# Kernel tuning notes

Measured on AMD Instinct MI355X. Metric: run time of the kernel, lower is better.

The kernel has to match this reference:

```python
import jax, jax.numpy as jnp
import numpy as np

N_NODES = 50000
N_EDGES = 400000


def setup_inputs() -> dict:
    key = jax.random.key(0)
    ks = jax.random.split(key, 8)
    d_in, d_hid, d_out = 512, 512, 256
    feats = jax.random.normal(ks[0], (N_NODES, d_in), dtype=jnp.float32)
    src = jax.random.randint(ks[1], (N_EDGES,), 0, N_NODES, dtype=jnp.int32)
    dst = jax.random.randint(ks[2], (N_EDGES,), 0, N_NODES, dtype=jnp.int32)
    # Glorot-ish scaled weights so activations stay O(1)
    W0 = jax.random.normal(ks[3], (d_in, d_hid), dtype=jnp.float32) / np.sqrt(d_in)
    b0 = jnp.zeros((d_hid,), jnp.float32)
    W1 = jax.random.normal(ks[4], (d_hid, d_hid), dtype=jnp.float32) / np.sqrt(d_hid)
    b1 = jnp.zeros((d_hid,), jnp.float32)
    W2 = jax.random.normal(ks[5], (d_hid, d_out), dtype=jnp.float32) / np.sqrt(d_hid)
    b2 = jnp.zeros((d_out,), jnp.float32)
    return {"feats": feats, "src": src, "dst": dst,
            "W0": W0, "b0": b0, "W1": W1, "b1": b1, "W2": W2, "b2": b2}


def _sage_conv_gcn(h, src, dst, W, b, deg):
    # DGL SAGEConv aggregator_type='gcn':
    # h_neigh[v] = (sum_{u->v} h[u] + h[v]) / (in_deg(v) + 1); out = h_neigh @ W + b
    agg = jax.ops.segment_sum(h[src], dst, num_segments=h.shape[0])  # [N, d]
    h_neigh = (agg + h) / (deg[:, None] + 1.0)
    return h_neigh @ W + b


def reference(feats, src, dst, W0, b0, W1, b1, W2, b2):
    N = feats.shape[0]
    deg = jax.ops.segment_sum(jnp.ones((src.shape[0],), feats.dtype), dst,
                              num_segments=N)  # in-degree per node
    h = jax.nn.relu(_sage_conv_gcn(feats, src, dst, W0, b0, deg))  # dropout p=0, norm none
    h = jax.nn.relu(_sage_conv_gcn(h, src, dst, W1, b1, deg))
    h = _sage_conv_gcn(h, src, dst, W2, b2, deg)  # final layer: no activation
    return h
```

## Files before the change

kernel.cpp:

```cpp
#include <hip/hip_runtime.h>
#include <stdint.h>

#define N_NODES 50000
#define N_EDGES 400000
#define MPAD    50048
#define SCAN_B  49

typedef __bf16 bf16x8 __attribute__((ext_vector_type(8)));
typedef float  f32x4  __attribute__((ext_vector_type(4)));
typedef unsigned short ushort_t;
typedef unsigned int   uint_t;

__device__ __forceinline__ ushort_t f2b(float f){
    uint_t x = __float_as_uint(f);
    x += 0x7FFFu + ((x >> 16) & 1u);
    return (ushort_t)(x >> 16);
}
__device__ __forceinline__ float b2f(ushort_t h){
    return __uint_as_float(((uint_t)h) << 16);
}

__global__ void zero_two(int* a, int* b, int n){
    int i = blockIdx.x * blockDim.x + threadIdx.x;
    if (i < n){ a[i] = 0; b[i] = 0; }
}

__global__ void hist_kernel(const int* __restrict__ dst, int* __restrict__ deg, int E){
    int i = blockIdx.x * blockDim.x + threadIdx.x;
    if (i < E) atomicAdd(&deg[dst[i]], 1);
}

__global__ __launch_bounds__(1024) void blk_scan_kernel(
        const int* __restrict__ deg, int* __restrict__ offs,
        int* __restrict__ bsum, int n){
    __shared__ int buf[1024];
    const int t = threadIdx.x, b = blockIdx.x;
    const int i = b * 1024 + t;
    int v = (i < n) ? deg[i] : 0;
    buf[t] = v; __syncthreads();
    for (int off = 1; off < 1024; off <<= 1){
        int x = (t >= off) ? buf[t - off] : 0;
        __syncthreads();
        buf[t] += x;
        __syncthreads();
    }
    if (i < n) offs[i] = buf[t] - v;
    if (t == 1023) bsum[b] = buf[1023];
}

__global__ void bsum_scan_kernel(int* __restrict__ bsum, int nb){
    int t = threadIdx.x;
    int orig = (t < nb) ? bsum[t] : 0;
    int v = orig;
    #pragma unroll
    for (int off = 1; off < 64; off <<= 1){
        int x = __shfl_up(v, off, 64);
        if (t >= off) v += x;
    }
    if (t < nb) bsum[t] = v - orig;
}

__global__ __launch_bounds__(1024) void add_off_kernel(
        int* __restrict__ offs, const int* __restrict__ bsum, int n){
    int i = blockIdx.x * 1024 + threadIdx.x;
    if (i < n) offs[i] += bsum[blockIdx.x];
    if (i == 0) offs[n] = N_EDGES;
}

__global__ void fill_kernel(const int* __restrict__ src, const int* __restrict__ dst,
                            const int* __restrict__ offs, int* __restrict__ cursor,
                            int* __restrict__ nbr, int E){
    int i = blockIdx.x * blockDim.x + threadIdx.x;
    if (i < E){
        int d = dst[i];
        int p = atomicAdd(&cursor[d], 1);
        nbr[offs[d] + p] = src[i];
    }
}

__global__ void f2b_kernel(const float4* __restrict__ in, ushort4* __restrict__ out, int n4){
    int i = blockIdx.x * blockDim.x + threadIdx.x;
    if (i < n4){
        float4 v = in[i];
        ushort4 o; o.x = f2b(v.x); o.y = f2b(v.y); o.z = f2b(v.z); o.w = f2b(v.w);
        out[i] = o;
    }
}

__global__ void wtrans_kernel(const float* __restrict__ W, ushort_t* __restrict__ Wt,
                              int K, int N){
    int i = blockIdx.x * blockDim.x + threadIdx.x;
    if (i < K * N){
        int n = i / K, k = i - n * K;
        Wt[i] = f2b(W[k * N + n]);
    }
}

__device__ __forceinline__ void load16(const void* g, void* l){
    __builtin_amdgcn_global_load_lds((const __attribute__((address_space(1))) void*)g,
                                     (__attribute__((address_space(3))) void*)l, 16, 0, 0);
}

__global__ __launch_bounds__(256, 2) void gemm_bt(const ushort_t* __restrict__ A,
                                                  const ushort_t* __restrict__ Bt,
                                                  ushort_t* __restrict__ C,
                                                  int N, int K){
    __shared__ ushort_t As[128 * 32];
    __shared__ ushort_t Bs[256 * 32];
    const int tid  = threadIdx.x, lane = tid & 63, wave = tid >> 6;
    const int bm = blockIdx.x, bn = blockIdx.y;
    const int fr = lane & 15;
    const int fk = (lane >> 4) * 8;
    const int wm = (wave >> 1) * 64, wn = (wave & 1) * 128;
    f32x4 acc[4][8] = {};

    for (int kt = 0; kt < K; kt += 32){
        __syncthreads();
        #pragma unroll
        for (int i = 0; i < 2; i++){
            int s = tid + i * 256;
            load16(A + (size_t)(bm * 128 + (s >> 2)) * K + kt + (s & 3) * 8,
                   (char*)As + s * 16);
        }
        #pragma unroll
        for (int i = 0; i < 4; i++){
            int s = tid + i * 256;
            load16(Bt + (size_t)(bn * 256 + (s >> 2)) * K + kt + (s & 3) * 8,
                   (char*)Bs + s * 16);
        }
        __syncthreads();
        bf16x8 af[4], bf[8];
        #pragma unroll
        for (int t = 0; t < 4; t++)
            af[t] = *(const bf16x8*)(const void*)(As + (wm + t * 16 + fr) * 32 + fk);
        #pragma unroll
        for (int t = 0; t < 8; t++)
            bf[t] = *(const bf16x8*)(const void*)(Bs + (wn + t * 16 + fr) * 32 + fk);
        #pragma unroll
        for (int tm = 0; tm < 4; tm++)
            #pragma unroll
            for (int tn = 0; tn < 8; tn++)
                acc[tm][tn] = __builtin_amdgcn_mfma_f32_16x16x32_bf16(
                                  af[tm], bf[tn], acc[tm][tn], 0, 0, 0);
    }
    const int r0 = (lane >> 4) * 4, c0 = lane & 15;
    #pragma unroll
    for (int tm = 0; tm < 4; tm++){
        #pragma unroll
        for (int tn = 0; tn < 8; tn++){
            int rbase = bm * 128 + wm + tm * 16 + r0;
            int cidx  = bn * 256 + wn + tn * 16 + c0;
            #pragma unroll
            for (int reg = 0; reg < 4; reg++)
                C[(size_t)(rbase + reg) * N + cidx] = f2b(acc[tm][tn][reg]);
        }
    }
}

__device__ __forceinline__ void acc8(float* a, uint4 y){
    a[0] += b2f((ushort_t)(y.x & 0xffff)); a[1] += b2f((ushort_t)(y.x >> 16));
    a[2] += b2f((ushort_t)(y.y & 0xffff)); a[3] += b2f((ushort_t)(y.y >> 16));
    a[4] += b2f((ushort_t)(y.z & 0xffff)); a[5] += b2f((ushort_t)(y.z >> 16));
    a[6] += b2f((ushort_t)(y.w & 0xffff)); a[7] += b2f((ushort_t)(y.w >> 16));
}
__device__ __forceinline__ void acc4(float* a, uint2 y){
    a[0] += b2f((ushort_t)(y.x & 0xffff)); a[1] += b2f((ushort_t)(y.x >> 16));
    a[2] += b2f((ushort_t)(y.y & 0xffff)); a[3] += b2f((ushort_t)(y.y >> 16));
}

__global__ __launch_bounds__(256) void agg_relu_kernel(
        const ushort_t* __restrict__ Y, const int* __restrict__ offs,
        const int* __restrict__ nbr, const float* __restrict__ bias,
        ushort_t* __restrict__ H){
    const int lane = threadIdx.x & 63, wave = threadIdx.x >> 6;
    const int v = blockIdx.x * 4 + wave;
    const int off = lane * 8;
    float a[8];
    {   uint4 y = *(const uint4*)(const void*)(Y + (size_t)v * 512 + off);
        a[0] = b2f((ushort_t)(y.x & 0xffff)); a[1] = b2f((ushort_t)(y.x >> 16));
        a[2] = b2f((ushort_t)(y.y & 0xffff)); a[3] = b2f((ushort_t)(y.y >> 16));
        a[4] = b2f((ushort_t)(y.z & 0xffff)); a[5] = b2f((ushort_t)(y.z >> 16));
        a[6] = b2f((ushort_t)(y.w & 0xffff)); a[7] = b2f((ushort_t)(y.w >> 16)); }
    const int beg = offs[v], end = offs[v + 1];
    int i = beg;
    for (; i + 8 <= end; i += 8){
        uint4 yy[8];
        #pragma unroll
        for (int j = 0; j < 8; j++){
            int u = nbr[i + j];
            yy[j] = *(const uint4*)(const void*)(Y + (size_t)u * 512 + off);
        }
        #pragma unroll
        for (int j = 0; j < 8; j++) acc8(a, yy[j]);
    }
    for (; i + 4 <= end; i += 4){
        uint4 yy[4];
        #pragma unroll
        for (int j = 0; j < 4; j++){
            int u = nbr[i + j];
            yy[j] = *(const uint4*)(const void*)(Y + (size_t)u * 512 + off);
        }
        #pragma unroll
        for (int j = 0; j < 4; j++) acc8(a, yy[j]);
    }
    for (; i < end; i++){
        int u = nbr[i];
        uint4 y = *(const uint4*)(const void*)(Y + (size_t)u * 512 + off);
        acc8(a, y);
    }
    const float inv = 1.0f / (float)(end - beg + 1);
    float4 bb0 = ((const float4*)bias)[lane * 2];
    float4 bb1 = ((const float4*)bias)[lane * 2 + 1];
    float r[8];
    r[0] = a[0]*inv + bb0.x; r[1] = a[1]*inv + bb0.y;
    r[2] = a[2]*inv + bb0.z; r[3] = a[3]*inv + bb0.w;
    r[4] = a[4]*inv + bb1.x; r[5] = a[5]*inv + bb1.y;
    r[6] = a[6]*inv + bb1.z; r[7] = a[7]*inv + bb1.w;
    #pragma unroll
    for (int j = 0; j < 8; j++) r[j] = r[j] > 0.f ? r[j] : 0.f;
    uint4 o;
    o.x = (uint_t)f2b(r[0]) | ((uint_t)f2b(r[1]) << 16);
    o.y = (uint_t)f2b(r[2]) | ((uint_t)f2b(r[3]) << 16);
    o.z = (uint_t)f2b(r[4]) | ((uint_t)f2b(r[5]) << 16);
    o.w = (uint_t)f2b(r[6]) | ((uint_t)f2b(r[7]) << 16);
    *(uint4*)(void*)(H + (size_t)v * 512 + off) = o;
}

__global__ __launch_bounds__(256) void agg_out_kernel(
        const ushort_t* __restrict__ Y, const int* __restrict__ offs,
        const int* __restrict__ nbr, const float* __restrict__ bias,
        float* __restrict__ out){
    const int lane = threadIdx.x & 63, wave = threadIdx.x >> 6;
    const int v = blockIdx.x * 4 + wave;
    const int off = lane * 4;
    float a[4];
    {   uint2 y = *(const uint2*)(const void*)(Y + (size_t)v * 256 + off);
        a[0] = b2f((ushort_t)(y.x & 0xffff)); a[1] = b2f((ushort_t)(y.x >> 16));
        a[2] = b2f((ushort_t)(y.y & 0xffff)); a[3] = b2f((ushort_t)(y.y >> 16)); }
    const int beg = offs[v], end = offs[v + 1];
    int i = beg;
    for (; i + 8 <= end; i += 8){
        uint2 yy[8];
        #pragma unroll
        for (int j = 0; j < 8; j++){
            int u = nbr[i + j];
            yy[j] = *(const uint2*)(const void*)(Y + (size_t)u * 256 + off);
        }
        #pragma unroll
        for (int j = 0; j < 8; j++) acc4(a, yy[j]);
    }
    for (; i + 4 <= end; i += 4){
        uint2 yy[4];
        #pragma unroll
        for (int j = 0; j < 4; j++){
            int u = nbr[i + j];
            yy[j] = *(const uint2*)(const void*)(Y + (size_t)u * 256 + off);
        }
        #pragma unroll
        for (int j = 0; j < 4; j++) acc4(a, yy[j]);
    }
    for (; i < end; i++){
        int u = nbr[i];
        uint2 y = *(const uint2*)(const void*)(Y + (size_t)u * 256 + off);
        acc4(a, y);
    }
    const float inv = 1.0f / (float)(end - beg + 1);
    float4 bb = ((const float4*)bias)[lane];
    float4 r;
    r.x = a[0]*inv + bb.x; r.y = a[1]*inv + bb.y;
    r.z = a[2]*inv + bb.z; r.w = a[3]*inv + bb.w;
    ((float4*)out)[v * 64 + lane] = r;
}

extern "C" void kernel_launch(void* const* d_in, const int* in_sizes, int n_in,
                              void* d_out, int out_size, void* d_ws, size_t ws_size,
                              hipStream_t stream) {
    const float* feats = (const float*)d_in[0];
    const int*   src   = (const int*)  d_in[1];
    const int*   dst   = (const int*)  d_in[2];
    const float* W0    = (const float*)d_in[3];
    const float* b0    = (const float*)d_in[4];
    const float* W1    = (const float*)d_in[5];
    const float* b1    = (const float*)d_in[6];
    const float* W2    = (const float*)d_in[7];
    const float* b2    = (const float*)d_in[8];
    float* out = (float*)d_out;

    char* w = (char*)d_ws;
    ushort_t* Abuf = (ushort_t*)w;  w += (size_t)MPAD * 512 * 2;
    ushort_t* Ybuf = (ushort_t*)w;  w += (size_t)MPAD * 512 * 2;
    ushort_t* W0t  = (ushort_t*)w;  w += 512 * 512 * 2;
    ushort_t* W1t  = (ushort_t*)w;  w += 512 * 512 * 2;
    ushort_t* W2t  = (ushort_t*)w;  w += 256 * 512 * 2;
    int* deg    = (int*)w;          w += 50048 * 4;
    int* offs   = (int*)w;          w += 50056 * 4;
    int* cursor = (int*)w;          w += 50048 * 4;
    int* nbr    = (int*)w;          w += (size_t)N_EDGES * 4;
    int* bsum   = (int*)w;          w += 64 * 4;

    zero_two<<<(N_NODES + 255) / 256, 256, 0, stream>>>(deg, cursor, N_NODES);
    hist_kernel<<<(N_EDGES + 255) / 256, 256, 0, stream>>>(dst, deg, N_EDGES);
    blk_scan_kernel<<<SCAN_B, 1024, 0, stream>>>(deg, offs, bsum, N_NODES);
    bsum_scan_kernel<<<1, 64, 0, stream>>>(bsum, SCAN_B);
    add_off_kernel<<<SCAN_B, 1024, 0, stream>>>(offs, bsum, N_NODES);
    fill_kernel<<<(N_EDGES + 255) / 256, 256, 0, stream>>>(src, dst, offs, cursor, nbr, N_EDGES);

    int n4 = N_NODES * 512 / 4;
    f2b_kernel<<<(n4 + 255) / 256, 256, 0, stream>>>((const float4*)feats, (ushort4*)Abuf, n4);
    wtrans_kernel<<<(512 * 512 + 255) / 256, 256, 0, stream>>>(W0, W0t, 512, 512);
    wtrans_kernel<<<(512 * 512 + 255) / 256, 256, 0, stream>>>(W1, W1t, 512, 512);
    wtrans_kernel<<<(512 * 256 + 255) / 256, 256, 0, stream>>>(W2, W2t, 512, 256);

    dim3 g01(MPAD / 128, 512 / 256);
    dim3 g2 (MPAD / 128, 256 / 256);

    gemm_bt<<<g01, 256, 0, stream>>>(Abuf, W0t, Ybuf, 512, 512);
    agg_relu_kernel<<<N_NODES / 4, 256, 0, stream>>>(Ybuf, offs, nbr, b0, Abuf);
    gemm_bt<<<g01, 256, 0, stream>>>(Abuf, W1t, Ybuf, 512, 512);
    agg_relu_kernel<<<N_NODES / 4, 256, 0, stream>>>(Ybuf, offs, nbr, b1, Abuf);
    gemm_bt<<<g2, 256, 0, stream>>>(Abuf, W2t, Ybuf, 256, 512);
    agg_out_kernel<<<N_NODES / 4, 256, 0, stream>>>(Ybuf, offs, nbr, b2, out);
}
```

Measured before the change: 517.2 us.

## Fuse fp32-to-bf16 conversion into first GEMM and retile GEMMs and aggregation

Removes the standalone feature conversion kernel by having the first GEMM read fp32 features directly and convert them to bf16 while staging into shared memory. The two 512-wide GEMMs move to a 64x512 tile so each block covers the full output width and reads each A row once. The relu aggregation kernel now splits each node across two waves with 8-byte loads, which raises the number of in-flight gathers per node. In exchange, the first GEMM does synchronous register loads and conversion instead of async global-to-LDS copies, and the larger B tile uses more shared memory per block.

```diff
diff --git a/kernel.cpp b/kernel.cpp
--- a/kernel.cpp
+++ b/kernel.cpp
@@ -78,15 +78,6 @@
     }
 }
 
-__global__ void f2b_kernel(const float4* __restrict__ in, ushort4* __restrict__ out, int n4){
-    int i = blockIdx.x * blockDim.x + threadIdx.x;
-    if (i < n4){
-        float4 v = in[i];
-        ushort4 o; o.x = f2b(v.x); o.y = f2b(v.y); o.z = f2b(v.z); o.w = f2b(v.w);
-        out[i] = o;
-    }
-}
-
 __global__ void wtrans_kernel(const float* __restrict__ W, ushort_t* __restrict__ Wt,
                               int K, int N){
     int i = blockIdx.x * blockDim.x + threadIdx.x;
@@ -99,6 +90,126 @@
 __device__ __forceinline__ void load16(const void* g, void* l){
     __builtin_amdgcn_global_load_lds((const __attribute__((address_space(1))) void*)g,
                                      (__attribute__((address_space(3))) void*)l, 16, 0, 0);
+}
+
+__global__ __launch_bounds__(256, 2) void gemm_bt512(const ushort_t* __restrict__ A,
+                                                     const ushort_t* __restrict__ Bt,
+                                                     ushort_t* __restrict__ C,
+                                                     int K){
+    __shared__ ushort_t As[64 * 32];
+    __shared__ ushort_t Bs[512 * 32];
+    const int tid  = threadIdx.x, lane = tid & 63, wave = tid >> 6;
+    const int bm = blockIdx.x;
+    const int fr = lane & 15;
+    const int fk = (lane >> 4) * 8;
+    const int wn = wave * 128;
+    f32x4 acc[4][8] = {};
+
+    for (int kt = 0; kt < K; kt += 32){
+        __syncthreads();
+        {
+            int s = tid;
+            load16(A + (size_t)(bm * 64 + (s >> 2)) * K + kt + (s & 3) * 8,
+                   (char*)As + s * 16);
+        }
+        #pragma unroll
+        for (int i = 0; i < 8; i++){
+            int s = tid + i * 256;
+            load16(Bt + (size_t)(s >> 2) * K + kt + (s & 3) * 8,
+                   (char*)Bs + s * 16);
+        }
+        __syncthreads();
+        bf16x8 af[4], bf[8];
+        #pragma unroll
+        for (int t = 0; t < 4; t++)
+            af[t] = *(const bf16x8*)(const void*)(As + (t * 16 + fr) * 32 + fk);
+        #pragma unroll
+        for (int t = 0; t < 8; t++)
+            bf[t] = *(const bf16x8*)(const void*)(Bs + (wn + t * 16 + fr) * 32 + fk);
+        #pragma unroll
+        for (int tm = 0; tm < 4; tm++)
+            #pragma unroll
+            for (int tn = 0; tn < 8; tn++)
+                acc[tm][tn] = __builtin_amdgcn_mfma_f32_16x16x32_bf16(
+                                  af[tm], bf[tn], acc[tm][tn], 0, 0, 0);
+    }
+    const int r0 = (lane >> 4) * 4, c0 = lane & 15;
+    #pragma unroll
+    for (int tm = 0; tm < 4; tm++){
+        #pragma unroll
+        for (int tn = 0; tn < 8; tn++){
+            int rbase = bm * 64 + tm * 16 + r0;
+            int cidx  = wn + tn * 16 + c0;
+            #pragma unroll
+            for (int reg = 0; reg < 4; reg++)
+                C[(size_t)(rbase + reg) * 512 + cidx] = f2b(acc[tm][tn][reg]);
+        }
+    }
+}
+
+__global__ __launch_bounds__(256, 2) void gemm_a32(const float* __restrict__ A,
+                                                   const ushort_t* __restrict__ Bt,
+                                                   ushort_t* __restrict__ C,
+                                                   int K){
+    __shared__ ushort_t As[64 * 32];
+    __shared__ ushort_t Bs[512 * 32];
+    const int tid  = threadIdx.x, lane = tid & 63, wave = tid >> 6;
+    const int bm = blockIdx.x;
+    const int fr = lane & 15;
+    const int fk = (lane >> 4) * 8;
+    const int wn = wave * 128;
+    f32x4 acc[4][8] = {};
+
+    for (int kt = 0; kt < K; kt += 32){
+        __syncthreads();
+        #pragma unroll
+        for (int i = 0; i < 8; i++){
+            int s = tid + i * 256;
+            load16(Bt + (size_t)(s >> 2) * K + kt + (s & 3) * 8,
+                   (char*)Bs + s * 16);
+        }
+        {
+            int s = tid;
+            int row = bm * 64 + (s >> 2);
+            uint4 o = make_uint4(0u, 0u, 0u, 0u);
+            if (row < N_NODES){
+                const float* p = A + (size_t)row * K + kt + (s & 3) * 8;
+                float4 x = *(const float4*)(const void*)p;
+                float4 y = *(const float4*)(const void*)(p + 4);
+                o.x = (uint_t)f2b(x.x) | ((uint_t)f2b(x.y) << 16);
+                o.y = (uint_t)f2b(x.z) | ((uint_t)f2b(x.w) << 16);
+                o.z = (uint_t)f2b(y.x) | ((uint_t)f2b(y.y) << 16);
+                o.w = (uint_t)f2b(y.z) | ((uint_t)f2b(y.w) << 16);
+            }
+            *(uint4*)(void*)((char*)As + s * 16) = o;
+        }
+        __syncthreads();
+        bf16x8 af[4], bf[8];
+        #pragma unroll
+        for (int t = 0; t < 4; t++)
+            af[t] = *(const bf16x8*)(const void*)(As + (t * 16 + fr) * 32 + fk);
+        #pragma unroll
+        for (int t = 0; t < 8; t++)
+            bf[t] = *(const bf16x8*)(const void*)(Bs + (wn + t * 16 + fr) * 32 + fk);
+        #pragma unroll
+        for (int tm = 0; tm < 4; tm++)
+            #pragma unroll
+            for (int tn = 0; tn < 8; tn++)
+                acc[tm][tn] = __builtin_amdgcn_mfma_f32_16x16x32_bf16(
+                                  af[tm], bf[tn], acc[tm][tn], 0, 0, 0);
+    }
+    const int r0 = (lane >> 4) * 4, c0 = lane & 15;
+    #pragma unroll
+    for (int tm = 0; tm < 4; tm++){
+        #pragma unroll
+        for (int tn = 0; tn < 8; tn++){
+            int rbase = bm * 64 + tm * 16 + r0;
+            int cidx  = wn + tn * 16 + c0;
+            #pragma unroll
+            for (int reg = 0; reg < 4; reg++)
+                C[(size_t)(rbase + reg) * 512 + cidx] = f2b(acc[tm][tn][reg]);
+        }
+    }
 }
 
 __global__ __launch_bounds__(256, 2) void gemm_bt(const ushort_t* __restrict__ A,
@@ -168,62 +279,55 @@
     a[2] += b2f((ushort_t)(y.y & 0xffff)); a[3] += b2f((ushort_t)(y.y >> 16));
 }
 
-__global__ __launch_bounds__(256) void agg_relu_kernel(
+__global__ __launch_bounds__(512) void agg_relu_kernel(
         const ushort_t* __restrict__ Y, const int* __restrict__ offs,
         const int* __restrict__ nbr, const float* __restrict__ bias,
         ushort_t* __restrict__ H){
-    const int lane = threadIdx.x & 63, wave = threadIdx.x >> 6;
-    const int v = blockIdx.x * 4 + wave;
-    const int off = lane * 8;
-    float a[8];
-    {   uint4 y = *(const uint4*)(const void*)(Y + (size_t)v * 512 + off);
+    const int lane = threadIdx.x & 63, wv = threadIdx.x >> 6;
+    const int v   = blockIdx.x * 4 + (wv >> 1);
+    const int off = (wv & 1) * 256 + lane * 4;
+    float a[4];
+    {   uint2 y = *(const uint2*)(const void*)(Y + (size_t)v * 512 + off);
         a[0] = b2f((ushort_t)(y.x & 0xffff)); a[1] = b2f((ushort_t)(y.x >> 16));
-        a[2] = b2f((ushort_t)(y.y & 0xffff)); a[3] = b2f((ushort_t)(y.y >> 16));
-        a[4] = b2f((ushort_t)(y.z & 0xffff)); a[5] = b2f((ushort_t)(y.z >> 16));
-        a[6] = b2f((ushort_t)(y.w & 0xffff)); a[7] = b2f((ushort_t)(y.w >> 16)); }
+        a[2] = b2f((ushort_t)(y.y & 0xffff)); a[3] = b2f((ushort_t)(y.y >> 16)); }
     const int beg = offs[v], end = offs[v + 1];
     int i = beg;
     for (; i + 8 <= end; i += 8){
-        uint4 yy[8];
+        uint2 yy[8];
         #pragma unroll
         for (int j = 0; j < 8; j++){
             int u = nbr[i + j];
-            yy[j] = *(const uint4*)(const void*)(Y + (size_t)u * 512 + off);
-        }
-        #pragma unroll
-        for (int j = 0; j < 8; j++) acc8(a, yy[j]);
+            yy[j] = *(const uint2*)(const void*)(Y + (size_t)u * 512 + off);
+        }
+        #pragma unroll
+        for (int j = 0; j < 8; j++) acc4(a, yy[j]);
     }
     for (; i + 4 <= end; i += 4){
-        uint4 yy[4];
+        uint2 yy[4];
         #pragma unroll
         for (int j = 0; j < 4; j++){
             int u = nbr[i + j];
-            yy[j] = *(const uint4*)(const void*)(Y + (size_t)u * 512 + off);
-        }
-        #pragma unroll
-        for (int j = 0; j < 4; j++) acc8(a, yy[j]);
+            yy[j] = *(const uint2*)(const void*)(Y + (size_t)u * 512 + off);
+        }
+        #pragma unroll
+        for (int j = 0; j < 4; j++) acc4(a, yy[j]);
     }
     for (; i < end; i++){
         int u = nbr[i];
-        uint4 y = *(const uint4*)(const void*)(Y + (size_t)u * 512 + off);
-        acc8(a, y);
+        uint2 y = *(const uint2*)(const void*)(Y + (size_t)u * 512 + off);
+        acc4(a, y);
     }
     const float inv = 1.0f / (float)(end - beg + 1);
-    float4 bb0 = ((const float4*)bias)[lane * 2];
-    float4 bb1 = ((const float4*)bias)[lane * 2 + 1];
-    float r[8];
-    r[0] = a[0]*inv + bb0.x; r[1] = a[1]*inv + bb0.y;
-    r[2] = a[2]*inv + bb0.z; r[3] = a[3]*inv + bb0.w;
-    r[4] = a[4]*inv + bb1.x; r[5] = a[5]*inv + bb1.y;
-    r[6] = a[6]*inv + bb1.z; r[7] = a[7]*inv + bb1.w;
+    float4 bb = ((const float4*)bias)[(wv & 1) * 64 + lane];
+    float r[4];
+    r[0] = a[0]*inv + bb.x; r[1] = a[1]*inv + bb.y;
+    r[2] = a[2]*inv + bb.z; r[3] = a[3]*inv + bb.w;
     #pragma unroll
-    for (int j = 0; j < 8; j++) r[j] = r[j] > 0.f ? r[j] : 0.f;
-    uint4 o;
+    for (int j = 0; j < 4; j++) r[j] = r[j] > 0.f ? r[j] : 0.f;
+    uint2 o;
     o.x = (uint_t)f2b(r[0]) | ((uint_t)f2b(r[1]) << 16);
     o.y = (uint_t)f2b(r[2]) | ((uint_t)f2b(r[3]) << 16);
-    o.z = (uint_t)f2b(r[4]) | ((uint_t)f2b(r[5]) << 16);
-    o.w = (uint_t)f2b(r[6]) | ((uint_t)f2b(r[7]) << 16);
-    *(uint4*)(void*)(H + (size_t)v * 512 + off) = o;
+    *(uint2*)(void*)(H + (size_t)v * 512 + off) = o;
 }
 
 __global__ __launch_bounds__(256) void agg_out_kernel(
@@ -305,19 +409,15 @@
     add_off_kernel<<<SCAN_B, 1024, 0, stream>>>(offs, bsum, N_NODES);
     fill_kernel<<<(N_EDGES + 255) / 256, 256, 0, stream>>>(src, dst, offs, cursor, nbr, N_EDGES);
 
-    int n4 = N_NODES * 512 / 4;
-    f2b_kernel<<<(n4 + 255) / 256, 256, 0, stream>>>((const float4*)feats, (ushort4*)Abuf, n4);
     wtrans_kernel<<<(512 * 512 + 255) / 256, 256, 0, stream>>>(W0, W0t, 512, 512);
     wtrans_kernel<<<(512 * 512 + 255) / 256, 256, 0, stream>>>(W1, W1t, 512, 512);
     wtrans_kernel<<<(512 * 256 + 255) / 256, 256, 0, stream>>>(W2, W2t, 512, 256);
 
-    dim3 g01(MPAD / 128, 512 / 256);
-    dim3 g2 (MPAD / 128, 256 / 256);
-
-    gemm_bt<<<g01, 256, 0, stream>>>(Abuf, W0t, Ybuf, 512, 512);
-    agg_relu_kernel<<<N_NODES / 4, 256, 0, stream>>>(Ybuf, offs, nbr, b0, Abuf);
-    gemm_bt<<<g01, 256, 0, stream>>>(Abuf, W1t, Ybuf, 512, 512);
-    agg_relu_kernel<<<N_NODES / 4, 256, 0, stream>>>(Ybuf, offs, nbr, b1, Abuf);
+    gemm_a32<<<MPAD / 64, 256, 0, stream>>>(feats, W0t, Ybuf, 512);
+    agg_relu_kernel<<<N_NODES / 4, 512, 0, stream>>>(Ybuf, offs, nbr, b0, Abuf);
+    gemm_bt512<<<MPAD / 64, 256, 0, stream>>>(Abuf, W1t, Ybuf, 512);
+    agg_relu_kernel<<<N_NODES / 4, 512, 0, stream>>>(Ybuf, offs, nbr, b1, Abuf);
+    dim3 g2(MPAD / 128, 1);
     gemm_bt<<<g2, 256, 0, stream>>>(Abuf, W2t, Ybuf, 256, 512);
     agg_out_kernel<<<N_NODES / 4, 256, 0, stream>>>(Ybuf, offs, nbr, b2, out);
 }
```

After: 519.1 us. About the same (+0.4%).

## Double-buffer GEMMs with swizzled LDS, XCD remap, and fused fp32-to-bf16 input

Applied to the files above, without the earlier changes.

Replaces the single-buffered 128x256 GEMM with a 128x128-tile, double-buffered LDS GEMM that uses an XOR swizzle to cut bank conflicts and remaps block IDs so neighbouring tiles share an XCD's L2. The first layer's GEMM now reads fp32 features directly and converts them to bf16 in registers, which removes the separate conversion kernel and its extra full-size round trip through memory. Smaller tiles raise occupancy and give more blocks, but they also reload A and B more often per output.

```diff
diff --git a/kernel.cpp b/kernel.cpp
--- a/kernel.cpp
+++ b/kernel.cpp
@@ -18,6 +18,13 @@
 }
 __device__ __forceinline__ float b2f(ushort_t h){
     return __uint_as_float(((uint_t)h) << 16);
+}
+
+__device__ __forceinline__ int xcd_swz(int orig, int nwg){
+    int q = nwg >> 3, r = nwg & 7;
+    int xcd = orig & 7, idx = orig >> 3;
+    int base = (xcd < r) ? xcd * (q + 1) : r * (q + 1) + (xcd - r) * q;
+    return base + idx;
 }
 
 __global__ void zero_two(int* a, int* b, int n){
@@ -78,15 +85,6 @@
     }
 }
 
-__global__ void f2b_kernel(const float4* __restrict__ in, ushort4* __restrict__ out, int n4){
-    int i = blockIdx.x * blockDim.x + threadIdx.x;
-    if (i < n4){
-        float4 v = in[i];
-        ushort4 o; o.x = f2b(v.x); o.y = f2b(v.y); o.z = f2b(v.z); o.w = f2b(v.w);
-        out[i] = o;
-    }
-}
-
 __global__ void wtrans_kernel(const float* __restrict__ W, ushort_t* __restrict__ Wt,
                               int K, int N){
     int i = blockIdx.x * blockDim.x + threadIdx.x;
@@ -101,58 +99,164 @@
                                      (__attribute__((address_space(3))) void*)l, 16, 0, 0);
 }
 
-__global__ __launch_bounds__(256, 2) void gemm_bt(const ushort_t* __restrict__ A,
-                                                  const ushort_t* __restrict__ Bt,
-                                                  ushort_t* __restrict__ C,
-                                                  int N, int K){
-    __shared__ ushort_t As[128 * 32];
-    __shared__ ushort_t Bs[256 * 32];
+__global__ __launch_bounds__(256, 4) void gemm128_bt(const ushort_t* __restrict__ A,
+                                                     const ushort_t* __restrict__ Bt,
+                                                     ushort_t* __restrict__ C,
+                                                     int NBN, int N, int K){
+    __shared__ ushort_t As[2][128 * 32];
+    __shared__ ushort_t Bs[2][128 * 32];
     const int tid  = threadIdx.x, lane = tid & 63, wave = tid >> 6;
-    const int bm = blockIdx.x, bn = blockIdx.y;
+    const int wg = xcd_swz(blockIdx.x, gridDim.x);
+    const int bm = wg / NBN, bn = wg - bm * NBN;
     const int fr = lane & 15;
-    const int fk = (lane >> 4) * 8;
-    const int wm = (wave >> 1) * 64, wn = (wave & 1) * 128;
-    f32x4 acc[4][8] = {};
-
-    for (int kt = 0; kt < K; kt += 32){
-        __syncthreads();
-        #pragma unroll
-        for (int i = 0; i < 2; i++){
-            int s = tid + i * 256;
-            load16(A + (size_t)(bm * 128 + (s >> 2)) * K + kt + (s & 3) * 8,
-                   (char*)As + s * 16);
-        }
-        #pragma unroll
-        for (int i = 0; i < 4; i++){
-            int s = tid + i * 256;
-            load16(Bt + (size_t)(bn * 256 + (s >> 2)) * K + kt + (s & 3) * 8,
-                   (char*)Bs + s * 16);
-        }
-        __syncthreads();
-        bf16x8 af[4], bf[8];
-        #pragma unroll
-        for (int t = 0; t < 4; t++)
-            af[t] = *(const bf16x8*)(const void*)(As + (wm + t * 16 + fr) * 32 + fk);
-        #pragma unroll
-        for (int t = 0; t < 8; t++)
-            bf[t] = *(const bf16x8*)(const void*)(Bs + (wn + t * 16 + fr) * 32 + fk);
+    const int wm = (wave >> 1) * 64, wn = (wave & 1) * 64;
+    f32x4 acc[4][4] = {};
+
+    const ushort_t* Ab = A  + (size_t)(bm * 128) * K;
+    const ushort_t* Bb = Bt + (size_t)(bn * 128) * K;
+
+    const int s0 = tid, s1 = tid + 256;
+    const int r0s = s0 >> 2, c0s = (s0 & 3) ^ ((r0s >> 1) & 3);
+    const int r1s = s1 >> 2, c1s = (s1 & 3) ^ ((r1s >> 1) & 3);
+
+    auto stage = [&](int kt, int pb){
+        load16(Ab + (size_t)r0s * K + kt + c0s * 8, (char*)As[pb] + s0 * 16);
+        load16(Ab + (size_t)r1s * K + kt + c1s * 8, (char*)As[pb] + s1 * 16);
+        load16(Bb + (size_t)r0s * K + kt + c0s * 8, (char*)Bs[pb] + s0 * 16);
+        load16(Bb + (size_t)r1s * K + kt + c1s * 8, (char*)Bs[pb] + s1 * 16);
+    };
+
+    stage(0, 0);
+    __syncthreads();
+    const int NT = K >> 5;
+    for (int t = 0; t < NT; ++t){
+        const int cur = t & 1;
+        if (t + 1 < NT) stage((t + 1) << 5, cur ^ 1);
+        __builtin_amdgcn_sched_barrier(0);
+        bf16x8 af[4], bf[4];
+        #pragma unroll
+        for (int q = 0; q < 4; q++){
+            int row = wm + q * 16 + fr;
+            int cx  = (lane >> 4) ^ ((row >> 1) & 3);
+            af[q] = *(const bf16x8*)(const void*)(&As[cur][row * 32 + cx * 8]);
+        }
+        #pragma unroll
+        for (int q = 0; q < 4; q++){
+            int row = wn + q * 16 + fr;
+            int cx  = (lane >> 4) ^ ((row >> 1) & 3);
+            bf[q] = *(const bf16x8*)(const void*)(&Bs[cur][row * 32 + cx * 8]);
+        }
         #pragma unroll
         for (int tm = 0; tm < 4; tm++)
             #pragma unroll
-            for (int tn = 0; tn < 8; tn++)
+            for (int tn = 0; tn < 4; tn++)
                 acc[tm][tn] = __builtin_amdgcn_mfma_f32_16x16x32_bf16(
                                   af[tm], bf[tn], acc[tm][tn], 0, 0, 0);
+        __syncthreads();
     }
     const int r0 = (lane >> 4) * 4, c0 = lane & 15;
     #pragma unroll
     for (int tm = 0; tm < 4; tm++){
         #pragma unroll
-        for (int tn = 0; tn < 8; tn++){
+        for (int tn = 0; tn < 4; tn++){
             int rbase = bm * 128 + wm + tm * 16 + r0;
-            int cidx  = bn * 256 + wn + tn * 16 + c0;
+            int cidx  = bn * 128 + wn + tn * 16 + c0;
             #pragma unroll
             for (int reg = 0; reg < 4; reg++)
                 C[(size_t)(rbase + reg) * N + cidx] = f2b(acc[tm][tn][reg]);
+        }
+    }
+}
+
+__global__ __launch_bounds__(256, 3) void gemm128_a32(const float* __restrict__ A,
+                                                      const ushort_t* __restrict__ Bt,
+                                                      ushort_t* __restrict__ C,
+                                                      int K){
+    __shared__ ushort_t As[2][128 * 32];
+    __shared__ ushort_t Bs[2][128 * 32];
+    const int tid  = threadIdx.x, lane = tid & 63, wave = tid >> 6;
+    const int wg = xcd_swz(blockIdx.x, gridDim.x);
+    const int bm = wg >> 2, bn = wg & 3;
+    const int fr = lane & 15;
+    const int wm = (wave >> 1) * 64, wn = (wave & 1) * 64;
+    f32x4 acc[4][4] = {};
+
+    const ushort_t* Bb = Bt + (size_t)(bn * 128) * K;
+    const int s0 = tid, s1 = tid + 256;
+    const int r0s = s0 >> 2, c0s = (s0 & 3) ^ ((r0s >> 1) & 3);
+    const int r1s = s1 >> 2, c1s = (s1 & 3) ^ ((r1s >> 1) & 3);
+    const int g0 = bm * 128 + r0s, g1 = bm * 128 + r1s;
+
+    float4 x0, y0, x1, y1;
+    auto loadA = [&](int kt){
+        if (g0 < N_NODES){
+            const float* p = A + (size_t)g0 * K + kt + c0s * 8;
+            x0 = *(const float4*)(const void*)p;
+            y0 = *(const float4*)(const void*)(p + 4);
+        } else { x0 = make_float4(0,0,0,0); y0 = make_float4(0,0,0,0); }
+        if (g1 < N_NODES){
+            const float* p = A + (size_t)g1 * K + kt + c1s * 8;
+            x1 = *(const float4*)(const void*)p;
+            y1 = *(const float4*)(const void*)(p + 4);
+        } else { x1 = make_float4(0,0,0,0); y1 = make_float4(0,0,0,0); }
+    };
+    auto stageB = [&](int kt, int pb){
+        load16(Bb + (size_t)r0s * K + kt + c0s * 8, (char*)Bs[pb] + s0 * 16);
+        load16(Bb + (size_t)r1s * K + kt + c1s * 8, (char*)Bs[pb] + s1 * 16);
+    };
+    auto writeA = [&](int pb){
+        uint4 o;
+        o.x = (uint_t)f2b(x0.x) | ((uint_t)f2b(x0.y) << 16);
+        o.y = (uint_t)f2b(x0.z) | ((uint_t)f2b(x0.w) << 16);
+        o.z = (uint_t)f2b(y0.x) | ((uint_t)f2b(y0.y) << 16);
+        o.w = (uint_t)f2b(y0.z) | ((uint_t)f2b(y0.w) << 16);
+        *(uint4*)(void*)((char*)As[pb] + s0 * 16) = o;
+        o.x = (uint_t)f2b(x1.x) | ((uint_t)f2b(x1.y) << 16);
+        o.y = (uint_t)f2b(x1.z) | ((uint_t)f2b(x1.w) << 16);
+        o.z = (uint_t)f2b(y1.x) | ((uint_t)f2b(y1.y) << 16);
+        o.w = (uint_t)f2b(y1.z) | ((uint_t)f2b(y1.w) << 16);
+        *(uint4*)(void*)((char*)As[pb] + s1 * 16) = o;
+    };
+
+    loadA(0); stageB(0, 0); writeA(0);
+    __syncthreads();
+    const int NT = K >> 5;
+    for (int t = 0; t < NT; ++t){
+        const int cur = t & 1;
+        if (t + 1 < NT){ loadA((t + 1) << 5); stageB((t + 1) << 5, cur ^ 1); }
+        __builtin_amdgcn_sched_barrier(0);
+        bf16x8 af[4], bf[4];
+        #pragma unroll
+        for (int q = 0; q < 4; q++){
+            int row = wm + q * 16 + fr;
+            int cx  = (lane >> 4) ^ ((row >> 1) & 3);
+            af[q] = *(const bf16x8*)(const void*)(&As[cur][row * 32 + cx * 8]);
+        }
+        #pragma unroll
+        for (int q = 0; q < 4; q++){
+            int row = wn + q * 16 + fr;
+            int cx  = (lane >> 4) ^ ((row >> 1) & 3);
+            bf[q] = *(const bf16x8*)(const void*)(&Bs[cur][row * 32 + cx * 8]);
+        }
+        #pragma unroll
+        for (int tm = 0; tm < 4; tm++)
+            #pragma unroll
+            for (int tn = 0; tn < 4; tn++)
+                acc[tm][tn] = __builtin_amdgcn_mfma_f32_16x16x32_bf16(
+                                  af[tm], bf[tn], acc[tm][tn], 0, 0, 0);
+        if (t + 1 < NT) writeA(cur ^ 1);
+        __syncthreads();
+    }
+    const int r0 = (lane >> 4) * 4, c0 = lane & 15;
+    #pragma unroll
+    for (int tm = 0; tm < 4; tm++){
+        #pragma unroll
+        for (int tn = 0; tn < 4; tn++){
+            int rbase = bm * 128 + wm + tm * 16 + r0;
+            int cidx  = bn * 128 + wn + tn * 16 + c0;
+            #pragma unroll
+            for (int reg = 0; reg < 4; reg++)
+                C[(size_t)(rbase + reg) * 512 + cidx] = f2b(acc[tm][tn][reg]);
         }
     }
 }
@@ -305,19 +409,17 @@
     add_off_kernel<<<SCAN_B, 1024, 0, stream>>>(offs, bsum, N_NODES);
     fill_kernel<<<(N_EDGES + 255) / 256, 256, 0, stream>>>(src, dst, offs, cursor, nbr, N_EDGES);
 
-    int n4 = N_NODES * 512 / 4;
-    f2b_kernel<<<(n4 + 255) / 256, 256, 0, stream>>>((const float4*)feats, (ushort4*)Abuf, n4);
     wtrans_kernel<<<(512 * 512 + 255) / 256, 256, 0, stream>>>(W0, W0t, 512, 512);
     wtrans_kernel<<<(512 * 512 + 255) / 256, 256, 0, stream>>>(W1, W1t, 512, 512);
     wtrans_kernel<<<(512 * 256 + 255) / 256, 256, 0, stream>>>(W2, W2t, 512, 256);
 
-    dim3 g01(MPAD / 128, 512 / 256);
-    dim3 g2 (MPAD / 128, 256 / 256);
-
-    gemm_bt<<<g01, 256, 0, stream>>>(Abuf, W0t, Ybuf, 512, 512);
+    const int g01 = (MPAD / 128) * 4;
+    const int g2  = (MPAD / 128) * 2;
+
+    gemm128_a32<<<g01, 256, 0, stream>>>(feats, W0t, Ybuf, 512);
     agg_relu_kernel<<<N_NODES / 4, 256, 0, stream>>>(Ybuf, offs, nbr, b0, Abuf);
-    gemm_bt<<<g01, 256, 0, stream>>>(Abuf, W1t, Ybuf, 512, 512);
+    gemm128_bt<<<g01, 256, 0, stream>>>(Abuf, W1t, Ybuf, 4, 512, 512);
     agg_relu_kernel<<<N_NODES / 4, 256, 0, stream>>>(Ybuf, offs, nbr, b1, Abuf);
-    gemm_bt<<<g2, 256, 0, stream>>>(Abuf, W2t, Ybuf, 256, 512);
+    gemm128_bt<<<g2, 256, 0, stream>>>(Abuf, W2t, Ybuf, 2, 256, 512);
     agg_out_kernel<<<N_NODES / 4, 256, 0, stream>>>(Ybuf, offs, nbr, b2, out);
 }
```

Result: no change. 514.4 us (-0.5%).

## Fuse fp32-to-bf16 input cast into first GEMM and use direct-load GEMMs

Applied to the files above, without the earlier changes.

Drops the separate feature-conversion kernel and folds the fp32-to-bf16 cast into the first GEMM, which reads fp32 features directly from global memory. The GEMMs move from LDS-staged 128x256 tiles to 128x128 tiles that load MFMA fragments straight from global memory into registers. Blocks are remapped with an XCD-aware swizzle for L2 locality, and weight transposition now goes through a shared-memory tile for coalescing. The catch is redundant global/L2 reads with no LDS reuse, plus the first GEMM reading twice the bytes for A.

```diff
diff --git a/kernel.cpp b/kernel.cpp
--- a/kernel.cpp
+++ b/kernel.cpp
@@ -5,6 +5,7 @@
 #define N_EDGES 400000
 #define MPAD    50048
 #define SCAN_B  49
+#define GK      512
 
 typedef __bf16 bf16x8 __attribute__((ext_vector_type(8)));
 typedef float  f32x4  __attribute__((ext_vector_type(4)));
@@ -18,6 +19,13 @@
 }
 __device__ __forceinline__ float b2f(ushort_t h){
     return __uint_as_float(((uint_t)h) << 16);
+}
+
+__device__ __forceinline__ int xcd_swz(int orig, int nwg){
+    int q = nwg >> 3, r = nwg & 7;
+    int xcd = orig & 7, idx = orig >> 3;
+    int base = (xcd < r) ? xcd * (q + 1) : r * (q + 1) + (xcd - r) * q;
+    return base + idx;
 }
 
 __global__ void zero_two(int* a, int* b, int n){
@@ -78,68 +86,50 @@
     }
 }
 
-__global__ void f2b_kernel(const float4* __restrict__ in, ushort4* __restrict__ out, int n4){
-    int i = blockIdx.x * blockDim.x + threadIdx.x;
-    if (i < n4){
-        float4 v = in[i];
-        ushort4 o; o.x = f2b(v.x); o.y = f2b(v.y); o.z = f2b(v.z); o.w = f2b(v.w);
-        out[i] = o;
-    }
-}
-
-__global__ void wtrans_kernel(const float* __restrict__ W, ushort_t* __restrict__ Wt,
-                              int K, int N){
-    int i = blockIdx.x * blockDim.x + threadIdx.x;
-    if (i < K * N){
-        int n = i / K, k = i - n * K;
-        Wt[i] = f2b(W[k * N + n]);
-    }
-}
-
-__device__ __forceinline__ void load16(const void* g, void* l){
-    __builtin_amdgcn_global_load_lds((const __attribute__((address_space(1))) void*)g,
-                                     (__attribute__((address_space(3))) void*)l, 16, 0, 0);
-}
-
-__global__ __launch_bounds__(256, 2) void gemm_bt(const ushort_t* __restrict__ A,
-                                                  const ushort_t* __restrict__ Bt,
-                                                  ushort_t* __restrict__ C,
-                                                  int N, int K){
-    __shared__ ushort_t As[128 * 32];
-    __shared__ ushort_t Bs[256 * 32];
-    const int tid  = threadIdx.x, lane = tid & 63, wave = tid >> 6;
-    const int bm = blockIdx.x, bn = blockIdx.y;
-    const int fr = lane & 15;
-    const int fk = (lane >> 4) * 8;
-    const int wm = (wave >> 1) * 64, wn = (wave & 1) * 128;
-    f32x4 acc[4][8] = {};
-
-    for (int kt = 0; kt < K; kt += 32){
-        __syncthreads();
-        #pragma unroll
-        for (int i = 0; i < 2; i++){
-            int s = tid + i * 256;
-            load16(A + (size_t)(bm * 128 + (s >> 2)) * K + kt + (s & 3) * 8,
-                   (char*)As + s * 16);
-        }
-        #pragma unroll
-        for (int i = 0; i < 4; i++){
-            int s = tid + i * 256;
-            load16(Bt + (size_t)(bn * 256 + (s >> 2)) * K + kt + (s & 3) * 8,
-                   (char*)Bs + s * 16);
-        }
-        __syncthreads();
-        bf16x8 af[4], bf[8];
-        #pragma unroll
-        for (int t = 0; t < 4; t++)
-            af[t] = *(const bf16x8*)(const void*)(As + (wm + t * 16 + fr) * 32 + fk);
-        #pragma unroll
-        for (int t = 0; t < 8; t++)
-            bf[t] = *(const bf16x8*)(const void*)(Bs + (wn + t * 16 + fr) * 32 + fk);
+__global__ __launch_bounds__(256) void wtrans_kernel(const float* __restrict__ W,
+                                                     ushort_t* __restrict__ Wt,
+                                                     int K, int N){
+    __shared__ float t[32][33];
+    const int bx = blockIdx.x * 32;
+    const int by = blockIdx.y * 32;
+    const int x = threadIdx.x & 31, y = threadIdx.x >> 5;
+    #pragma unroll
+    for (int j = 0; j < 32; j += 8)
+        t[y + j][x] = W[(size_t)(by + y + j) * N + bx + x];
+    __syncthreads();
+    #pragma unroll
+    for (int j = 0; j < 32; j += 8)
+        Wt[(size_t)(bx + y + j) * K + by + x] = f2b(t[x][y + j]);
+}
+
+__global__ __launch_bounds__(256, 4) void gemm_dir_bt(const ushort_t* __restrict__ A,
+                                                      const ushort_t* __restrict__ Bt,
+                                                      ushort_t* __restrict__ C,
+                                                      int NBN, int N){
+    const int tid = threadIdx.x, lane = tid & 63, wave = tid >> 6;
+    const int wg = xcd_swz(blockIdx.x, gridDim.x);
+    const int bm = wg / NBN, bn = wg - bm * NBN;
+    const int fr = lane & 15, fk = (lane >> 4) * 8;
+    const int wm = (wave >> 1) * 64, wn = (wave & 1) * 64;
+    const ushort_t* Aq[4];
+    const ushort_t* Bq[4];
+    #pragma unroll
+    for (int q = 0; q < 4; q++){
+        Aq[q] = A  + (size_t)(bm * 128 + wm + q * 16 + fr) * GK + fk;
+        Bq[q] = Bt + (size_t)(bn * 128 + wn + q * 16 + fr) * GK + fk;
+    }
+    f32x4 acc[4][4] = {};
+    #pragma unroll 4
+    for (int kt = 0; kt < GK; kt += 32){
+        bf16x8 af[4], bf[4];
+        #pragma unroll
+        for (int q = 0; q < 4; q++) af[q] = *(const bf16x8*)(const void*)(Aq[q] + kt);
+        #pragma unroll
+        for (int q = 0; q < 4; q++) bf[q] = *(const bf16x8*)(const void*)(Bq[q] + kt);
         #pragma unroll
         for (int tm = 0; tm < 4; tm++)
             #pragma unroll
-            for (int tn = 0; tn < 8; tn++)
+            for (int tn = 0; tn < 4; tn++)
                 acc[tm][tn] = __builtin_amdgcn_mfma_f32_16x16x32_bf16(
                                   af[tm], bf[tn], acc[tm][tn], 0, 0, 0);
     }
@@ -147,12 +137,67 @@
     #pragma unroll
     for (int tm = 0; tm < 4; tm++){
         #pragma unroll
-        for (int tn = 0; tn < 8; tn++){
+        for (int tn = 0; tn < 4; tn++){
             int rbase = bm * 128 + wm + tm * 16 + r0;
-            int cidx  = bn * 256 + wn + tn * 16 + c0;
+            int cidx  = bn * 128 + wn + tn * 16 + c0;
             #pragma unroll
             for (int reg = 0; reg < 4; reg++)
                 C[(size_t)(rbase + reg) * N + cidx] = f2b(acc[tm][tn][reg]);
+        }
+    }
+}
+
+__global__ __launch_bounds__(256, 3) void gemm_dir_a32(const float* __restrict__ A,
+                                                       const ushort_t* __restrict__ Bt,
+                                                       ushort_t* __restrict__ C){
+    const int tid = threadIdx.x, lane = tid & 63, wave = tid >> 6;
+    const int wg = xcd_swz(blockIdx.x, gridDim.x);
+    const int bm = wg >> 2, bn = wg & 3;
+    const int fr = lane & 15, fk = (lane >> 4) * 8;
+    const int wm = (wave >> 1) * 64, wn = (wave & 1) * 64;
+    const float* Aq[4];
+    const ushort_t* Bq[4];
+    #pragma unroll
+    for (int q = 0; q < 4; q++){
+        int r = bm * 128 + wm + q * 16 + fr;
+        if (r > N_NODES - 1) r = N_NODES - 1;
+        Aq[q] = A  + (size_t)r * GK + fk;
+        Bq[q] = Bt + (size_t)(bn * 128 + wn + q * 16 + fr) * GK + fk;
+    }
+    f32x4 acc[4][4] = {};
+    #pragma unroll 2
+    for (int kt = 0; kt < GK; kt += 32){
+        bf16x8 af[4], bf[4];
+        #pragma unroll
+        for (int q = 0; q < 4; q++){
+            float4 x = *(const float4*)(const void*)(Aq[q] + kt);
+            float4 y = *(const float4*)(const void*)(Aq[q] + kt + 4);
+            uint4 o;
+            o.x = (uint_t)f2b(x.x) | ((uint_t)f2b(x.y) << 16);
+            o.y = (uint_t)f2b(x.z) | ((uint_t)f2b(x.w) << 16);
+            o.z = (uint_t)f2b(y.x) | ((uint_t)f2b(y.y) << 16);
+            o.w = (uint_t)f2b(y.z) | ((uint_t)f2b(y.w) << 16);
+            af[q] = *(bf16x8*)&o;
+        }
+        #pragma unroll
+        for (int q = 0; q < 4; q++) bf[q] = *(const bf16x8*)(const void*)(Bq[q] + kt);
+        #pragma unroll
+        for (int tm = 0; tm < 4; tm++)
+            #pragma unroll
+            for (int tn = 0; tn < 4; tn++)
+                acc[tm][tn] = __builtin_amdgcn_mfma_f32_16x16x32_bf16(
+                                  af[tm], bf[tn], acc[tm][tn], 0, 0, 0);
+    }
+    const int r0 = (lane >> 4) * 4, c0 = lane & 15;
+    #pragma unroll
+    for (int tm = 0; tm < 4; tm++){
+        #pragma unroll
+        for (int tn = 0; tn < 4; tn++){
+            int rbase = bm * 128 + wm + tm * 16 + r0;
+            int cidx  = bn * 128 + wn + tn * 16 + c0;
+            #pragma unroll
+            for (int reg = 0; reg < 4; reg++)
+                C[(size_t)(rbase + reg) * 512 + cidx] = f2b(acc[tm][tn][reg]);
         }
     }
 }
@@ -305,19 +350,21 @@
     add_off_kernel<<<SCAN_B, 1024, 0, stream>>>(offs, bsum, N_NODES);
     fill_kernel<<<(N_EDGES + 255) / 256, 256, 0, stream>>>(src, dst, offs, cursor, nbr, N_EDGES);
 
-    int n4 = N_NODES * 512 / 4;
-    f2b_kernel<<<(n4 + 255) / 256, 256, 0, stream>>>((const float4*)feats, (ushort4*)Abuf, n4);
-    wtrans_kernel<<<(512 * 512 + 255) / 256, 256, 0, stream>>>(W0, W0t, 512, 512);
-    wtrans_kernel<<<(512 * 512 + 255) / 256, 256, 0, stream>>>(W1, W1t, 512, 512);
-    wtrans_kernel<<<(512 * 256 + 255) / 256, 256, 0, stream>>>(W2, W2t, 512, 256);
-
-    dim3 g01(MPAD / 128, 512 / 256);
-    dim3 g2 (MPAD / 128, 256 / 256);
-
-    gemm_bt<<<g01, 256, 0, stream>>>(Abuf, W0t, Ybuf, 512, 512);
+    {
+        dim3 gt0(512 / 32, 512 / 32);
+        wtrans_kernel<<<gt0, 256, 0, stream>>>(W0, W0t, 512, 512);
+        wtrans_kernel<<<gt0, 256, 0, stream>>>(W1, W1t, 512, 512);
+        dim3 gt2(256 / 32, 512 / 32);
+        wtrans_kernel<<<gt2, 256, 0, stream>>>(W2, W2t, 512, 256);
+    }
+
+    const int g01 = (MPAD / 128) * 4;
+    const int g2  = (MPAD / 128) * 2;
+
+    gemm_dir_a32<<<g01, 256, 0, stream>>>(feats, W0t, Ybuf);
     agg_relu_kernel<<<N_NODES / 4, 256, 0, stream>>>(Ybuf, offs, nbr, b0, Abuf);
-    gemm_bt<<<g01, 256, 0, stream>>>(Abuf, W1t, Ybuf, 512, 512);
+    gemm_dir_bt<<<g01, 256, 0, stream>>>(Abuf, W1t, Ybuf, 4, 512);
     agg_relu_kernel<<<N_NODES / 4, 256, 0, stream>>>(Ybuf, offs, nbr, b1, Abuf);
-    gemm_bt<<<g2, 256, 0, stream>>>(Abuf, W2t, Ybuf, 256, 512);
+    gemm_dir_bt<<<g2, 256, 0, stream>>>(Abuf, W2t, Ybuf, 2, 256);
     agg_out_kernel<<<N_NODES / 4, 256, 0, stream>>>(Ybuf, offs, nbr, b2, out);
 }
```

Result: slower. 732.4 us (+41.6%).
